# Kernel tuning notes

Measured on AMD Instinct MI355X. Metric: run time of the kernel, lower is better.

Reference implementation:

```python
import jax, jax.numpy as jnp
import numpy as np

N = 8192       # number of points
C = 16         # num_colors (size of color distribution)
DIM = 2        # spatial dim (GeometricLoss(dim=2))


def setup_inputs() -> dict:
    key = jax.random.key(0)
    k1, k2 = jax.random.split(key)
    outputs = jax.random.normal(k1, (N, C), dtype=jnp.float32)
    points = jax.random.normal(k2, (N, DIM), dtype=jnp.float32)
    return {"outputs": outputs, "points": points, "k": 5}


def reference(outputs, points, k):
    # cdist(points, points) via the squared-norm expansion (avoids [N,N,dim] tensor)
    sq = jnp.sum(points * points, axis=1)                      # [N]
    d2 = sq[:, None] + sq[None, :] - 2.0 * (points @ points.T)  # [N,N]
    dist = jnp.sqrt(jnp.maximum(d2, 0.0))
    # k+1 smallest distances per row; drop self (distance 0)
    _, idx = jax.lax.top_k(-dist, k + 1)                        # [N,k+1]
    idx = idx[:, 1:]                                            # [N,k]
    neighbor_outputs = outputs[idx]                             # [N,k,C] gather
    # ||out_i - out_j|| over color dim, mean over all (i, neighbor) pairs
    differences = jnp.linalg.norm(outputs[:, None, :] - neighbor_outputs, axis=2)
    return differences.mean()
```

## Files before the change

kernel.cpp:

```cpp
#include <hip/hip_runtime.h>


static constexpr int NPTS    = 8192;
static constexpr int KNN     = 5;
static constexpr int CH      = 16;
static constexpr int QPB     = 8;
static constexpr int THREADS = 512;
static constexpr int NBLK    = NPTS / QPB;
static constexpr int CAP     = 128;
static constexpr int NF4     = NPTS / 2;
static constexpr int ITERS   = NF4 / THREADS;

__device__ __forceinline__ unsigned long long shfl_xor_u64(unsigned long long v, int m) {
    unsigned int lo = (unsigned int)v;
    unsigned int hi = (unsigned int)(v >> 32);
    lo = __shfl_xor(lo, m, 64);
    hi = __shfl_xor(hi, m, 64);
    return ((unsigned long long)hi << 32) | lo;
}

__device__ __forceinline__ float rfl(float x) {
    return __uint_as_float(__builtin_amdgcn_readfirstlane(__float_as_uint(x)));
}

__global__ __launch_bounds__(512, 2) void knn_loss_kernel(
        const float* __restrict__ outputs,
        const float* __restrict__ points,
        float* __restrict__ partial) {
    const int tid   = threadIdx.x;
    const int wave  = tid >> 6;
    const int lane  = tid & 63;
    const int qbase = blockIdx.x * QPB;

    const float2* __restrict__ pts2 = (const float2*)points;
    const float4* __restrict__ pts4 = (const float4*)points;
    const float FINF = __int_as_float(0x7f800000);

    float pix[QPB], piy[QPB];
    #pragma unroll
    for (int q = 0; q < QPB; ++q) {
        const float2 pq = pts2[qbase + q];
        pix[q] = rfl(pq.x); piy[q] = rfl(pq.y);
    }

    float4 p[ITERS];
    #pragma unroll
    for (int u = 0; u < ITERS; ++u)
        p[u] = pts4[u * THREADS + tid];

    float acc[QPB];
    #pragma unroll
    for (int q = 0; q < QPB; ++q) acc[q] = FINF;
    #pragma unroll
    for (int u = 0; u < ITERS; ++u) {
        #pragma unroll
        for (int q = 0; q < QPB; ++q) {
            const float dxa = pix[q] - p[u].x, dya = piy[q] - p[u].y;
            const float dxb = pix[q] - p[u].z, dyb = piy[q] - p[u].w;
            const float d2a = fmaf(dxa, dxa, dya * dya);
            const float d2b = fmaf(dxb, dxb, dyb * dyb);
            acc[q] = fminf(fminf(acc[q], d2a), d2b);
        }
    }

    __shared__ float thrmin[QPB][THREADS];
    __shared__ unsigned long long buf[QPB][CAP];
    __shared__ int cnt[QPB];
    __shared__ float Ts[QPB];
    __shared__ float red[QPB];

    #pragma unroll
    for (int q = 0; q < QPB; ++q)
        thrmin[q][tid] = fmaxf(acc[q], 0.0f);
    if (tid < QPB) cnt[tid] = 0;
    __syncthreads();

    {
        float v = thrmin[wave][lane];
        #pragma unroll
        for (int r = 1; r < THREADS / 64; ++r)
            v = fminf(v, thrmin[wave][lane + r * 64]);
        float T = 0.0f;
        #pragma unroll
        for (int t = 0; t < KNN + 1; ++t) {
            float m = v;
            #pragma unroll
            for (int d = 1; d < 64; d <<= 1) m = fminf(m, __shfl_xor(m, d, 64));
            if (v == m) v = FINF;
            T = m;
        }
        if (lane == 0) Ts[wave] = T;
    }
    __syncthreads();

    float Tq[QPB];
    #pragma unroll
    for (int q = 0; q < QPB; ++q) Tq[q] = rfl(Ts[q]);

    #pragma unroll
    for (int u = 0; u < ITERS; ++u) {
        const int jpair = u * THREADS + tid;
        #pragma unroll
        for (int q = 0; q < QPB; ++q) {
            const float dxa = pix[q] - p[u].x, dya = piy[q] - p[u].y;
            const float dxb = pix[q] - p[u].z, dyb = piy[q] - p[u].w;
            const float d2a = fmaf(dxa, dxa, dya * dya);
            const float d2b = fmaf(dxb, dxb, dyb * dyb);
            if (fminf(d2a, d2b) <= Tq[q]) {
                if (d2a <= Tq[q]) {
                    const int pos = atomicAdd(&cnt[q], 1);
                    if (pos < CAP)
                        buf[q][pos] =
                            ((unsigned long long)__float_as_uint(fmaxf(d2a, 0.0f)) << 32)
                            | (unsigned int)(2 * jpair);
                }
                if (d2b <= Tq[q]) {
                    const int pos = atomicAdd(&cnt[q], 1);
                    if (pos < CAP)
                        buf[q][pos] =
                            ((unsigned long long)__float_as_uint(fmaxf(d2b, 0.0f)) << 32)
                            | (unsigned int)(2 * jpair + 1);
                }
            }
        }
    }
    __syncthreads();

    const unsigned long long INF64 = ~0ull;
    const int n = min(cnt[wave], CAP);
    unsigned long long a  = (lane      < n) ? buf[wave][lane]      : INF64;
    unsigned long long b2 = (lane + 64 < n) ? buf[wave][lane + 64] : INF64;
    if (b2 < a) { unsigned long long t = a; a = b2; b2 = t; }

    unsigned int myj = 0;
    int active = 0;
    #pragma unroll
    for (int t = 0; t < KNN + 1; ++t) {
        unsigned long long m = a;
        #pragma unroll
        for (int d = 1; d < 64; d <<= 1) {
            const unsigned long long x = shfl_xor_u64(m, d);
            if (x < m) m = x;
        }
        if (a == m) { a = b2; b2 = INF64; }
        if (t >= 1 && lane == t) { myj = (unsigned int)m; active = 1; }
    }

    float nrm = 0.0f;
    if (active) {
        const float4* oi = (const float4*)(outputs + (size_t)(qbase + wave) * CH);
        const float4* oj = (const float4*)(outputs + (size_t)myj * CH);
        float s = 0.0f;
        #pragma unroll
        for (int c = 0; c < 4; ++c) {
            const float4 x = oi[c], y = oj[c];
            const float dx = x.x - y.x, dy = x.y - y.y;
            const float dz = x.z - y.z, dw = x.w - y.w;
            s += dx * dx + dy * dy + dz * dz + dw * dw;
        }
        nrm = sqrtf(s);
    }
    #pragma unroll
    for (int d = 1; d < 64; d <<= 1) nrm += __shfl_xor(nrm, d, 64);

    if (lane == 0) red[wave] = nrm;
    __syncthreads();
    if (tid == 0) {
        float s = 0.0f;
        #pragma unroll
        for (int wv = 0; wv < QPB; ++wv) s += red[wv];
        partial[blockIdx.x] = s;
    }
}

__global__ __launch_bounds__(256) void finalize_kernel(
        const float* __restrict__ partial, float* __restrict__ out) {
    double s = 0.0;
    for (int idx = threadIdx.x; idx < NBLK; idx += 256) s += (double)partial[idx];
    #pragma unroll
    for (int d = 1; d < 64; d <<= 1) s += __shfl_xor(s, d, 64);
    __shared__ double lds[4];
    const int wave = threadIdx.x >> 6;
    const int lane = threadIdx.x & 63;
    if (lane == 0) lds[wave] = s;
    __syncthreads();
    if (threadIdx.x == 0)
        out[0] = (float)((lds[0] + lds[1] + lds[2] + lds[3]) /
                         (double)((long long)NPTS * KNN));
}

extern "C" void kernel_launch(void* const* d_in, const int* in_sizes, int n_in,
                              void* d_out, int out_size, void* d_ws, size_t ws_size,
                              hipStream_t stream) {
    const float* outputs = (const float*)d_in[0];
    const float* points  = (const float*)d_in[1];
    float* partial = (float*)d_ws;
    float* out = (float*)d_out;

    knn_loss_kernel<<<NBLK, THREADS, 0, stream>>>(outputs, points, partial);
    finalize_kernel<<<1, 256, 0, stream>>>(partial, out);
}
```

Before: 99.94 us.

## Use half-norm minus dot-product distance expansion and shrink block to 4 queries

Replaces the per-pair squared-distance computation with the expansion e = 0.5*|p_j|^2 - p_i·p_j. The per-point half-norm is hoisted out of the query loop, so each pair needs two FMAs instead of subtract, multiply and FMA. The true squared distance is rebuilt only for candidates that pass the threshold. Block size also drops to 256 threads with 4 queries per block, which doubles the block count and the per-thread point registers. That means each thread rescans more points for fewer queries. Thresholds are now negative-capable, and cancellation in the expanded form could change which near-tied neighbors get selected.

```diff
diff --git a/kernel.cpp b/kernel.cpp
--- a/kernel.cpp
+++ b/kernel.cpp
@@ -4,8 +4,8 @@
 static constexpr int NPTS    = 8192;
 static constexpr int KNN     = 5;
 static constexpr int CH      = 16;
-static constexpr int QPB     = 8;
-static constexpr int THREADS = 512;
+static constexpr int QPB     = 4;
+static constexpr int THREADS = 256;
 static constexpr int NBLK    = NPTS / QPB;
 static constexpr int CAP     = 128;
 static constexpr int NF4     = NPTS / 2;
@@ -23,7 +23,7 @@
     return __uint_as_float(__builtin_amdgcn_readfirstlane(__float_as_uint(x)));
 }
 
-__global__ __launch_bounds__(512, 2) void knn_loss_kernel(
+__global__ __launch_bounds__(256, 2) void knn_loss_kernel(
         const float* __restrict__ outputs,
         const float* __restrict__ points,
         float* __restrict__ partial) {
@@ -36,11 +36,12 @@
     const float4* __restrict__ pts4 = (const float4*)points;
     const float FINF = __int_as_float(0x7f800000);
 
-    float pix[QPB], piy[QPB];
+    float pix[QPB], piy[QPB], sqi[QPB];
     #pragma unroll
     for (int q = 0; q < QPB; ++q) {
         const float2 pq = pts2[qbase + q];
         pix[q] = rfl(pq.x); piy[q] = rfl(pq.y);
+        sqi[q] = rfl(fmaf(pix[q], pix[q], piy[q] * piy[q]));
     }
 
     float4 p[ITERS];
@@ -53,13 +54,13 @@
     for (int q = 0; q < QPB; ++q) acc[q] = FINF;
     #pragma unroll
     for (int u = 0; u < ITERS; ++u) {
+        const float hA = 0.5f * fmaf(p[u].x, p[u].x, p[u].y * p[u].y);
+        const float hB = 0.5f * fmaf(p[u].z, p[u].z, p[u].w * p[u].w);
         #pragma unroll
         for (int q = 0; q < QPB; ++q) {
-            const float dxa = pix[q] - p[u].x, dya = piy[q] - p[u].y;
-            const float dxb = pix[q] - p[u].z, dyb = piy[q] - p[u].w;
-            const float d2a = fmaf(dxa, dxa, dya * dya);
-            const float d2b = fmaf(dxb, dxb, dyb * dyb);
-            acc[q] = fminf(fminf(acc[q], d2a), d2b);
+            const float eA = fmaf(-pix[q], p[u].x, fmaf(-piy[q], p[u].y, hA));
+            const float eB = fmaf(-pix[q], p[u].z, fmaf(-piy[q], p[u].w, hB));
+            acc[q] = fminf(fminf(acc[q], eA), eB);
         }
     }
 
@@ -71,7 +72,7 @@
 
     #pragma unroll
     for (int q = 0; q < QPB; ++q)
-        thrmin[q][tid] = fmaxf(acc[q], 0.0f);
+        thrmin[q][tid] = acc[q];
     if (tid < QPB) cnt[tid] = 0;
     __syncthreads();
 
@@ -100,26 +101,26 @@
     #pragma unroll
     for (int u = 0; u < ITERS; ++u) {
         const int jpair = u * THREADS + tid;
+        const float hA = 0.5f * fmaf(p[u].x, p[u].x, p[u].y * p[u].y);
+        const float hB = 0.5f * fmaf(p[u].z, p[u].z, p[u].w * p[u].w);
         #pragma unroll
         for (int q = 0; q < QPB; ++q) {
-            const float dxa = pix[q] - p[u].x, dya = piy[q] - p[u].y;
-            const float dxb = pix[q] - p[u].z, dyb = piy[q] - p[u].w;
-            const float d2a = fmaf(dxa, dxa, dya * dya);
-            const float d2b = fmaf(dxb, dxb, dyb * dyb);
-            if (fminf(d2a, d2b) <= Tq[q]) {
-                if (d2a <= Tq[q]) {
+            const float eA = fmaf(-pix[q], p[u].x, fmaf(-piy[q], p[u].y, hA));
+            const float eB = fmaf(-pix[q], p[u].z, fmaf(-piy[q], p[u].w, hB));
+            if (fminf(eA, eB) <= Tq[q]) {
+                if (eA <= Tq[q]) {
+                    const float d2 = fmaxf(fmaf(2.0f, eA, sqi[q]), 0.0f);
                     const int pos = atomicAdd(&cnt[q], 1);
                     if (pos < CAP)
-                        buf[q][pos] =
-                            ((unsigned long long)__float_as_uint(fmaxf(d2a, 0.0f)) << 32)
-                            | (unsigned int)(2 * jpair);
+                        buf[q][pos] = ((unsigned long long)__float_as_uint(d2) << 32)
+                                      | (unsigned int)(2 * jpair);
                 }
-                if (d2b <= Tq[q]) {
+                if (eB <= Tq[q]) {
+                    const float d2 = fmaxf(fmaf(2.0f, eB, sqi[q]), 0.0f);
                     const int pos = atomicAdd(&cnt[q], 1);
                     if (pos < CAP)
-                        buf[q][pos] =
-                            ((unsigned long long)__float_as_uint(fmaxf(d2b, 0.0f)) << 32)
-                            | (unsigned int)(2 * jpair + 1);
+                        buf[q][pos] = ((unsigned long long)__float_as_uint(d2) << 32)
+                                      | (unsigned int)(2 * jpair + 1);
                 }
             }
         }
```

Measured after the change: 90.04 us. 1.11x faster.
